# Kernel tuning notes

Hardware: AMD Instinct MI355X
Metric: run time of the kernel (lower is better)

## Reference

```python
import jax, jax.numpy as jnp
import numpy as np

BETA = 0.9
THRESHOLD = 1.0
SLOPE = 25.0  # snntorch fast_sigmoid default slope
T_STEPS = 64
IN_DIM, HID, NCLS = 256, 128, 8
BATCH = 16384


@jax.custom_vjp
def spike(u):
    # heaviside(u) with fast_sigmoid surrogate gradient
    return (u > 0).astype(u.dtype)

def _spike_fwd(u):
    return spike(u), u

def _spike_bwd(u, g):
    return (g / (SLOPE * jnp.abs(u) + 1.0) ** 2,)

spike.defvjp(_spike_fwd, _spike_bwd)


def setup_inputs() -> dict:
    key = jax.random.key(0)
    k1, k2, k3, k4, k5 = jax.random.split(key, 5)
    b1_bound = 1.0 / np.sqrt(IN_DIM)
    b2_bound = 1.0 / np.sqrt(HID)
    return {
        "x": jax.random.normal(k1, (BATCH, IN_DIM), jnp.float32),
        "W1": jax.random.uniform(k2, (HID, IN_DIM), jnp.float32, -b1_bound, b1_bound),
        "b1": jax.random.uniform(k3, (HID,), jnp.float32, -b1_bound, b1_bound),
        "W2": jax.random.uniform(k4, (NCLS, HID), jnp.float32, -b2_bound, b2_bound),
        "b2": jax.random.uniform(k5, (NCLS,), jnp.float32, -b2_bound, b2_bound),
    }


def reference(x, W1, b1, W2, b2):
    # fc1(x) is identical every timestep -> hoist out of the loop (same math)
    cur1 = x @ W1.T + b1  # [B, HID]

    def step(carry, _):
        mem1, mem2, acc = carry
        # snntorch Leaky (reset_mechanism='subtract'):
        # reset computed from incoming mem, detached
        reset1 = jax.lax.stop_gradient((mem1 - THRESHOLD > 0).astype(mem1.dtype))
        mem1 = BETA * mem1 + cur1 - reset1 * THRESHOLD
        spk1 = spike(mem1 - THRESHOLD)

        cur2 = spk1 @ W2.T + b2  # [B, NCLS]
        reset2 = jax.lax.stop_gradient((mem2 - THRESHOLD > 0).astype(mem2.dtype))
        mem2 = BETA * mem2 + cur2 - reset2 * THRESHOLD
        spk2 = spike(mem2 - THRESHOLD)
        return (mem1, mem2, acc + spk2), None

    mem1_0 = jnp.zeros((x.shape[0], HID), x.dtype)
    mem2_0 = jnp.zeros((x.shape[0], NCLS), x.dtype)
    acc0 = jnp.zeros((x.shape[0], NCLS), x.dtype)
    (_, _, out), _ = jax.lax.scan(step, (mem1_0, mem2_0, acc0), None, length=T_STEPS)
    return out
```

## Files before the change

kernel.cpp:

```cpp
#include <hip/hip_runtime.h>
#include <math.h>


#define T_STEPS 64
#define IN_DIM  256
#define HID     128
#define NCLS    8

#define ROWS   32
#define THR    256
#define A_KQ   16
#define RSTR   260

typedef float f32x4 __attribute__((ext_vector_type(4)));

static __device__ __forceinline__ unsigned int pkspk(float a, float b) {
    auto h = __builtin_amdgcn_cvt_pkrtz(a, b);
    return __builtin_bit_cast(unsigned int, h);
}

__global__ __launch_bounds__(THR, 2)
void snn_fused(const float* __restrict__ x, const float* __restrict__ W1,
               const float* __restrict__ b1, const float* __restrict__ W2,
               const float* __restrict__ b2, float* __restrict__ out)
{
#pragma clang fp contract(off)
    __shared__ __align__(16) char smem[33280];
    float4 (* const w1c)[HID + 2] = (float4 (*)[HID + 2])smem;
    unsigned int* const pk  = (unsigned int*)smem;
    float*        const wsl = (float*)smem;

    const int tid  = threadIdx.x;
    const int lane = tid & 63;

    {
        const int wv = __builtin_amdgcn_readfirstlane(tid >> 6);
        const size_t rowg0 = (size_t)blockIdx.x * ROWS;
        const float* xb = x + (rowg0 + (size_t)wv * 8) * IN_DIM;

        float accL[8], accH[8];
        #pragma unroll
        for (int j = 0; j < 8; ++j) { accL[j] = 0.0f; accH[j] = 0.0f; }

        #pragma unroll 1
        for (int ch = 0; ch < 4; ++ch) {
            const int kbase = ch * (A_KQ * 4);
            #pragma unroll
            for (int s = 0; s < 8; ++s) {
                const int idx = tid + s * THR;
                const int h = idx >> 4, kq = idx & 15;
                w1c[kq][h] = *(const float4*)(W1 + (size_t)h * IN_DIM + kbase + kq * 4);
            }
            __syncthreads();

            const float* xbc = xb + kbase;
            #pragma unroll 4
            for (int kq = 0; kq < A_KQ; ++kq) {
                const float* xkq = xbc + kq * 4;
                f32x4 q0, q1, q2, q3, q4, q5, q6, q7;
                asm volatile(
                    "s_load_dwordx4 %0, %8, 0x0\n\t"
                    "s_load_dwordx4 %1, %8, 0x400\n\t"
                    "s_load_dwordx4 %2, %8, 0x800\n\t"
                    "s_load_dwordx4 %3, %8, 0xc00\n\t"
                    "s_load_dwordx4 %4, %8, 0x1000\n\t"
                    "s_load_dwordx4 %5, %8, 0x1400\n\t"
                    "s_load_dwordx4 %6, %8, 0x1800\n\t"
                    "s_load_dwordx4 %7, %8, 0x1c00\n\t"
                    "s_waitcnt lgkmcnt(0)"
                    : "=&s"(q0), "=&s"(q1), "=&s"(q2), "=&s"(q3),
                      "=&s"(q4), "=&s"(q5), "=&s"(q6), "=&s"(q7)
                    : "s"(xkq));

                const float4 wL = w1c[kq][lane];
                const float4 wH = w1c[kq][64 + lane];
#define ROWFMA(J, XQ) { \
                float aL = accL[J], aH = accH[J]; \
                aL = fmaf(XQ.x, wL.x, aL); \
                aL = fmaf(XQ.y, wL.y, aL); \
                aL = fmaf(XQ.z, wL.z, aL); \
                aL = fmaf(XQ.w, wL.w, aL); \
                aH = fmaf(XQ.x, wH.x, aH); \
                aH = fmaf(XQ.y, wH.y, aH); \
                aH = fmaf(XQ.z, wH.z, aH); \
                aH = fmaf(XQ.w, wH.w, aH); \
                accL[J] = aL; accH[J] = aH; }
                ROWFMA(0, q0) ROWFMA(1, q1) ROWFMA(2, q2) ROWFMA(3, q3)
                ROWFMA(4, q4) ROWFMA(5, q5) ROWFMA(6, q6) ROWFMA(7, q7)
#undef ROWFMA
            }
            __syncthreads();
        }

        const float bL = b1[lane], bH = b1[64 + lane];
        #pragma unroll
        for (int j = 0; j < 8; ++j) {
            const int rr = wv * 8 + j;
            wsl[rr * HID + lane]      = accL[j] + bL;
            wsl[rr * HID + 64 + lane] = accH[j] + bH;
        }
    }

    const int r = tid >> 3;
    const int q = tid & 7;

    const int brow = lane & 31;
    const int bcls = 2 * (tid >> 6) + (lane >> 5);
    const float b2c = b2[bcls];

    float4 w2r[32];
    {
        const float4* wg = (const float4*)(W2 + bcls * HID);
        #pragma unroll
        for (int g = 0; g < 32; ++g) w2r[g] = wg[g];
    }

    __syncthreads();

    float cur1[16];
    {
        const float* src = wsl + r * HID + q * 16;
        #pragma unroll
        for (int i = 0; i < 4; ++i) {
            const float4 v = *(const float4*)(src + 4 * i);
            cur1[4*i+0] = v.x; cur1[4*i+1] = v.y;
            cur1[4*i+2] = v.z; cur1[4*i+3] = v.w;
        }
    }
    __syncthreads();

    float mem1[16], spk1[16];
    #pragma unroll
    for (int i = 0; i < 16; ++i) { mem1[i] = 0.0f; spk1[i] = 0.0f; }
    float m2 = 0.0f, r2v = 0.0f, o = 0.0f;

    #pragma unroll 1
    for (int ts = 0; ts < T_STEPS; ts += 4) {
        #pragma unroll
        for (int j = 0; j < 4; ++j) {
            #pragma unroll
            for (int i = 0; i < 16; ++i) {
                float tmp = 0.9f * mem1[i];
                tmp = tmp + cur1[i];
                float m = tmp - spk1[i];
                mem1[i] = m;
                spk1[i] = (m > 1.0f) ? 1.0f : 0.0f;
            }
            unsigned int* dst = &pk[r * RSTR + j * 64 + q * 8];
            #pragma unroll
            for (int s = 0; s < 2; ++s) {
                uint4 pv;
                pv.x = pkspk(spk1[8*s+0], spk1[8*s+1]);
                pv.y = pkspk(spk1[8*s+2], spk1[8*s+3]);
                pv.z = pkspk(spk1[8*s+4], spk1[8*s+5]);
                pv.w = pkspk(spk1[8*s+6], spk1[8*s+7]);
                *(uint4*)(dst + 4 * s) = pv;
            }
        }
        __syncthreads();

        float a0 = 0.0f, a1 = 0.0f, a2 = 0.0f, a3 = 0.0f;
        const unsigned int* src = &pk[brow * RSTR];
#define FMIX_LO(A, P, W) \
        asm("v_fma_mix_f32 %0, %1, %2, %0 op_sel_hi:[1,0,0]" \
            : "+v"(A) : "v"(P), "v"(W));
#define FMIX_HI(A, P, W) \
        asm("v_fma_mix_f32 %0, %1, %2, %0 op_sel:[1,0,0] op_sel_hi:[1,0,0]" \
            : "+v"(A) : "v"(P), "v"(W));
#define TR(A, P) \
        FMIX_LO(A, P.x, wA.x) FMIX_HI(A, P.x, wA.y) \
        FMIX_LO(A, P.y, wA.z) FMIX_HI(A, P.y, wA.w) \
        FMIX_LO(A, P.z, wB.x) FMIX_HI(A, P.z, wB.y) \
        FMIX_LO(A, P.w, wB.z) FMIX_HI(A, P.w, wB.w)
        #pragma unroll
        for (int gg = 0; gg < 16; ++gg) {
            const float4 wA = w2r[2 * gg];
            const float4 wB = w2r[2 * gg + 1];
            const uint4 p0 = *(const uint4*)(src + 0 * 64 + 4 * gg);
            const uint4 p1 = *(const uint4*)(src + 1 * 64 + 4 * gg);
            const uint4 p2 = *(const uint4*)(src + 2 * 64 + 4 * gg);
            const uint4 p3 = *(const uint4*)(src + 3 * 64 + 4 * gg);
            TR(a0, p0) TR(a1, p1) TR(a2, p2) TR(a3, p3)
        }
#undef TR
#undef FMIX_HI
#undef FMIX_LO
        __syncthreads();

        const float aa[4] = {a0, a1, a2, a3};
        #pragma unroll
        for (int j = 0; j < 4; ++j) {
            const float c2 = aa[j] + b2c;
            float t2 = 0.9f * m2; t2 = t2 + c2; m2 = t2 - r2v;
            r2v = (m2 > 1.0f) ? 1.0f : 0.0f;
            o = o + r2v;
        }
    }

    out[((size_t)blockIdx.x * ROWS + brow) * NCLS + bcls] = o;
}

extern "C" void kernel_launch(void* const* d_in, const int* in_sizes, int n_in,
                              void* d_out, int out_size, void* d_ws, size_t ws_size,
                              hipStream_t stream) {
    const float* x  = (const float*)d_in[0];
    const float* W1 = (const float*)d_in[1];
    const float* b1 = (const float*)d_in[2];
    const float* W2 = (const float*)d_in[3];
    const float* b2 = (const float*)d_in[4];
    float* out = (float*)d_out;
    (void)d_ws; (void)ws_size;

    const int batch = in_sizes[0] / IN_DIM;
    snn_fused<<<batch / ROWS, THR, 0, stream>>>(x, W1, b1, W2, b2, out);
}
```

Before: 144.6 us.

## Halve rows per block, stage W2 in LDS, split layer-2 timesteps across lane halves

Each block now handles 16 rows instead of 32, and the launch bound asks for 4 blocks per CU instead of 2. Per-thread state shrinks from 16 to 8 hidden neurons, and the 32-register W2 row cache moves into shared memory. The layer-2 reduction splits the four timesteps between lane halves, which exchange results with a cross-lane shuffle, and only half the lanes write output. The aim is lower register pressure and higher occupancy to hide latency. The cost is twice as many blocks, W1 reloaded per block, extra LDS reads of W2, and a shuffle each step.

```diff
diff --git a/kernel.cpp b/kernel.cpp
--- a/kernel.cpp
+++ b/kernel.cpp
@@ -7,7 +7,7 @@
 #define HID     128
 #define NCLS    8
 
-#define ROWS   32
+#define ROWS   16
 #define THR    256
 #define A_KQ   16
 #define RSTR   260
@@ -19,7 +19,7 @@
     return __builtin_bit_cast(unsigned int, h);
 }
 
-__global__ __launch_bounds__(THR, 2)
+__global__ __launch_bounds__(THR, 4)
 void snn_fused(const float* __restrict__ x, const float* __restrict__ W1,
                const float* __restrict__ b1, const float* __restrict__ W2,
                const float* __restrict__ b2, float* __restrict__ out)
@@ -28,6 +28,7 @@
     __shared__ __align__(16) char smem[33280];
     float4 (* const w1c)[HID + 2] = (float4 (*)[HID + 2])smem;
     unsigned int* const pk  = (unsigned int*)smem;
+    float4*       const w2l = (float4*)(smem + 16640);
     float*        const wsl = (float*)smem;
 
     const int tid  = threadIdx.x;
@@ -36,11 +37,11 @@
     {
         const int wv = __builtin_amdgcn_readfirstlane(tid >> 6);
         const size_t rowg0 = (size_t)blockIdx.x * ROWS;
-        const float* xb = x + (rowg0 + (size_t)wv * 8) * IN_DIM;
-
-        float accL[8], accH[8];
-        #pragma unroll
-        for (int j = 0; j < 8; ++j) { accL[j] = 0.0f; accH[j] = 0.0f; }
+        const float* xb = x + (rowg0 + (size_t)wv * 4) * IN_DIM;
+
+        float accL[4], accH[4];
+        #pragma unroll
+        for (int j = 0; j < 4; ++j) { accL[j] = 0.0f; accH[j] = 0.0f; }
 
         #pragma unroll 1
         for (int ch = 0; ch < 4; ++ch) {
@@ -57,19 +58,14 @@
             #pragma unroll 4
             for (int kq = 0; kq < A_KQ; ++kq) {
                 const float* xkq = xbc + kq * 4;
-                f32x4 q0, q1, q2, q3, q4, q5, q6, q7;
+                f32x4 q0, q1, q2, q3;
                 asm volatile(
-                    "s_load_dwordx4 %0, %8, 0x0\n\t"
-                    "s_load_dwordx4 %1, %8, 0x400\n\t"
-                    "s_load_dwordx4 %2, %8, 0x800\n\t"
-                    "s_load_dwordx4 %3, %8, 0xc00\n\t"
-                    "s_load_dwordx4 %4, %8, 0x1000\n\t"
-                    "s_load_dwordx4 %5, %8, 0x1400\n\t"
-                    "s_load_dwordx4 %6, %8, 0x1800\n\t"
-                    "s_load_dwordx4 %7, %8, 0x1c00\n\t"
+                    "s_load_dwordx4 %0, %4, 0x0\n\t"
+                    "s_load_dwordx4 %1, %4, 0x400\n\t"
+                    "s_load_dwordx4 %2, %4, 0x800\n\t"
+                    "s_load_dwordx4 %3, %4, 0xc00\n\t"
                     "s_waitcnt lgkmcnt(0)"
-                    : "=&s"(q0), "=&s"(q1), "=&s"(q2), "=&s"(q3),
-                      "=&s"(q4), "=&s"(q5), "=&s"(q6), "=&s"(q7)
+                    : "=&s"(q0), "=&s"(q1), "=&s"(q2), "=&s"(q3)
                     : "s"(xkq));
 
                 const float4 wL = w1c[kq][lane];
@@ -86,7 +82,6 @@
                 aH = fmaf(XQ.w, wH.w, aH); \
                 accL[J] = aL; accH[J] = aH; }
                 ROWFMA(0, q0) ROWFMA(1, q1) ROWFMA(2, q2) ROWFMA(3, q3)
-                ROWFMA(4, q4) ROWFMA(5, q5) ROWFMA(6, q6) ROWFMA(7, q7)
 #undef ROWFMA
             }
             __syncthreads();
@@ -94,34 +89,23 @@
 
         const float bL = b1[lane], bH = b1[64 + lane];
         #pragma unroll
-        for (int j = 0; j < 8; ++j) {
-            const int rr = wv * 8 + j;
+        for (int j = 0; j < 4; ++j) {
+            const int rr = wv * 4 + j;
             wsl[rr * HID + lane]      = accL[j] + bL;
             wsl[rr * HID + 64 + lane] = accH[j] + bH;
         }
+        w2l[tid] = ((const float4*)W2)[tid];
     }
-
-    const int r = tid >> 3;
-    const int q = tid & 7;
-
-    const int brow = lane & 31;
-    const int bcls = 2 * (tid >> 6) + (lane >> 5);
-    const float b2c = b2[bcls];
-
-    float4 w2r[32];
+    __syncthreads();
+
+    const int r = tid >> 4;
+    const int q = tid & 15;
+
+    float cur1[8];
     {
-        const float4* wg = (const float4*)(W2 + bcls * HID);
-        #pragma unroll
-        for (int g = 0; g < 32; ++g) w2r[g] = wg[g];
-    }
-
-    __syncthreads();
-
-    float cur1[16];
-    {
-        const float* src = wsl + r * HID + q * 16;
-        #pragma unroll
-        for (int i = 0; i < 4; ++i) {
+        const float* src = wsl + r * HID + q * 8;
+        #pragma unroll
+        for (int i = 0; i < 2; ++i) {
             const float4 v = *(const float4*)(src + 4 * i);
             cur1[4*i+0] = v.x; cur1[4*i+1] = v.y;
             cur1[4*i+2] = v.z; cur1[4*i+3] = v.w;
@@ -129,9 +113,16 @@
     }
     __syncthreads();
 
-    float mem1[16], spk1[16];
+    const int brow  = lane & 15;
+    const int u     = lane >> 4;
+    const bool hihalf = (lane >= 32);
+    const int bcls  = 2 * (tid >> 6) + (u & 1);
+    const float b2c = b2[bcls];
+    const float4* __restrict__ w2p = &w2l[bcls * 32];
+
+    float mem1[8], spk1[8];
     #pragma unroll
-    for (int i = 0; i < 16; ++i) { mem1[i] = 0.0f; spk1[i] = 0.0f; }
+    for (int i = 0; i < 8; ++i) { mem1[i] = 0.0f; spk1[i] = 0.0f; }
     float m2 = 0.0f, r2v = 0.0f, o = 0.0f;
 
     #pragma unroll 1
@@ -139,28 +130,24 @@
         #pragma unroll
         for (int j = 0; j < 4; ++j) {
             #pragma unroll
-            for (int i = 0; i < 16; ++i) {
+            for (int i = 0; i < 8; ++i) {
                 float tmp = 0.9f * mem1[i];
                 tmp = tmp + cur1[i];
                 float m = tmp - spk1[i];
                 mem1[i] = m;
                 spk1[i] = (m > 1.0f) ? 1.0f : 0.0f;
             }
-            unsigned int* dst = &pk[r * RSTR + j * 64 + q * 8];
-            #pragma unroll
-            for (int s = 0; s < 2; ++s) {
-                uint4 pv;
-                pv.x = pkspk(spk1[8*s+0], spk1[8*s+1]);
-                pv.y = pkspk(spk1[8*s+2], spk1[8*s+3]);
-                pv.z = pkspk(spk1[8*s+4], spk1[8*s+5]);
-                pv.w = pkspk(spk1[8*s+6], spk1[8*s+7]);
-                *(uint4*)(dst + 4 * s) = pv;
-            }
+            uint4 pv;
+            pv.x = pkspk(spk1[0], spk1[1]);
+            pv.y = pkspk(spk1[2], spk1[3]);
+            pv.z = pkspk(spk1[4], spk1[5]);
+            pv.w = pkspk(spk1[6], spk1[7]);
+            *(uint4*)(&pk[r * RSTR + j * 64 + q * 4]) = pv;
         }
         __syncthreads();
 
-        float a0 = 0.0f, a1 = 0.0f, a2 = 0.0f, a3 = 0.0f;
-        const unsigned int* src = &pk[brow * RSTR];
+        float aE = 0.0f, aF = 0.0f;
+        const unsigned int* srcT = &pk[brow * RSTR + (hihalf ? 128 : 0)];
 #define FMIX_LO(A, P, W) \
         asm("v_fma_mix_f32 %0, %1, %2, %0 op_sel_hi:[1,0,0]" \
             : "+v"(A) : "v"(P), "v"(W));
@@ -174,30 +161,35 @@
         FMIX_LO(A, P.w, wB.z) FMIX_HI(A, P.w, wB.w)
         #pragma unroll
         for (int gg = 0; gg < 16; ++gg) {
-            const float4 wA = w2r[2 * gg];
-            const float4 wB = w2r[2 * gg + 1];
-            const uint4 p0 = *(const uint4*)(src + 0 * 64 + 4 * gg);
-            const uint4 p1 = *(const uint4*)(src + 1 * 64 + 4 * gg);
-            const uint4 p2 = *(const uint4*)(src + 2 * 64 + 4 * gg);
-            const uint4 p3 = *(const uint4*)(src + 3 * 64 + 4 * gg);
-            TR(a0, p0) TR(a1, p1) TR(a2, p2) TR(a3, p3)
+            const float4 wA = w2p[2 * gg];
+            const float4 wB = w2p[2 * gg + 1];
+            const uint4 ra = *(const uint4*)(srcT + 4 * gg);
+            const uint4 rb = *(const uint4*)(srcT + 64 + 4 * gg);
+            TR(aE, ra) TR(aF, rb)
         }
 #undef TR
 #undef FMIX_HI
 #undef FMIX_LO
         __syncthreads();
 
-        const float aa[4] = {a0, a1, a2, a3};
+        const float pE = __shfl_xor(aE, 32, 64);
+        const float pF = __shfl_xor(aF, 32, 64);
+        const float t0 = hihalf ? pE : aE;
+        const float t1 = hihalf ? pF : aF;
+        const float t2 = hihalf ? aE : pE;
+        const float t3 = hihalf ? aF : pF;
+        const float aa[4] = {t0, t1, t2, t3};
         #pragma unroll
         for (int j = 0; j < 4; ++j) {
             const float c2 = aa[j] + b2c;
-            float t2 = 0.9f * m2; t2 = t2 + c2; m2 = t2 - r2v;
+            float tt = 0.9f * m2; tt = tt + c2; m2 = tt - r2v;
             r2v = (m2 > 1.0f) ? 1.0f : 0.0f;
             o = o + r2v;
         }
     }
 
-    out[((size_t)blockIdx.x * ROWS + brow) * NCLS + bcls] = o;
+    if (lane < 32)
+        out[((size_t)blockIdx.x * ROWS + brow) * NCLS + bcls] = o;
 }
 
 extern "C" void kernel_launch(void* const* d_in, const int* in_sizes, int n_in,
```

New measurement: 152.6 us. 1.05x slower.

## Double-buffer spike LDS buffer to overlap layer-1 update with layer-2 matvec

Applied to the files above, without the earlier changes.

Splits the packed spike buffer in shared memory into two halves and software-pipelines the time loop. Each iteration writes the next four timesteps' layer-1 spikes into one buffer while reading the current buffer for the layer-2 reduction, which halves the barriers per iteration. The cost is doubling LDS use to about 65 KB per block, which at launch bounds of two blocks per CU may lower occupancy. It also adds a prologue and a buffer-select branch.

```diff
diff --git a/kernel.cpp b/kernel.cpp
--- a/kernel.cpp
+++ b/kernel.cpp
@@ -25,9 +25,10 @@
                const float* __restrict__ b2, float* __restrict__ out)
 {
 #pragma clang fp contract(off)
-    __shared__ __align__(16) char smem[33280];
+    __shared__ __align__(16) char smem[66560];
     float4 (* const w1c)[HID + 2] = (float4 (*)[HID + 2])smem;
-    unsigned int* const pk  = (unsigned int*)smem;
+    unsigned int* const pkA = (unsigned int*)smem;
+    unsigned int* const pkB = (unsigned int*)(smem + 33280);
     float*        const wsl = (float*)smem;
 
     const int tid  = threadIdx.x;
@@ -134,33 +135,41 @@
     for (int i = 0; i < 16; ++i) { mem1[i] = 0.0f; spk1[i] = 0.0f; }
     float m2 = 0.0f, r2v = 0.0f, o = 0.0f;
 
+#define PHASE_A(BUF) \
+    _Pragma("unroll") \
+    for (int j = 0; j < 4; ++j) { \
+        _Pragma("unroll") \
+        for (int i = 0; i < 16; ++i) { \
+            float tmp = 0.9f * mem1[i];    \
+            tmp = tmp + cur1[i];           \
+            float m = tmp - spk1[i];       \
+            mem1[i] = m; \
+            spk1[i] = (m > 1.0f) ? 1.0f : 0.0f; \
+        } \
+        unsigned int* dst = &(BUF)[r * RSTR + j * 64 + q * 8]; \
+        _Pragma("unroll") \
+        for (int s = 0; s < 2; ++s) { \
+            uint4 pv; \
+            pv.x = pkspk(spk1[8*s+0], spk1[8*s+1]); \
+            pv.y = pkspk(spk1[8*s+2], spk1[8*s+3]); \
+            pv.z = pkspk(spk1[8*s+4], spk1[8*s+5]); \
+            pv.w = pkspk(spk1[8*s+6], spk1[8*s+7]); \
+            *(uint4*)(dst + 4 * s) = pv; \
+        } \
+    }
+
+    PHASE_A(pkA);
+    __syncthreads();
+
     #pragma unroll 1
-    for (int ts = 0; ts < T_STEPS; ts += 4) {
-        #pragma unroll
-        for (int j = 0; j < 4; ++j) {
-            #pragma unroll
-            for (int i = 0; i < 16; ++i) {
-                float tmp = 0.9f * mem1[i];
-                tmp = tmp + cur1[i];
-                float m = tmp - spk1[i];
-                mem1[i] = m;
-                spk1[i] = (m > 1.0f) ? 1.0f : 0.0f;
-            }
-            unsigned int* dst = &pk[r * RSTR + j * 64 + q * 8];
-            #pragma unroll
-            for (int s = 0; s < 2; ++s) {
-                uint4 pv;
-                pv.x = pkspk(spk1[8*s+0], spk1[8*s+1]);
-                pv.y = pkspk(spk1[8*s+2], spk1[8*s+3]);
-                pv.z = pkspk(spk1[8*s+4], spk1[8*s+5]);
-                pv.w = pkspk(spk1[8*s+6], spk1[8*s+7]);
-                *(uint4*)(dst + 4 * s) = pv;
-            }
-        }
-        __syncthreads();
+    for (int g = 0; g < 16; ++g) {
+        unsigned int* const curb = (g & 1) ? pkB : pkA;
+        unsigned int* const nxtb = (g & 1) ? pkA : pkB;
+
+        if (g < 15) { PHASE_A(nxtb); }
 
         float a0 = 0.0f, a1 = 0.0f, a2 = 0.0f, a3 = 0.0f;
-        const unsigned int* src = &pk[brow * RSTR];
+        const unsigned int* src = &curb[brow * RSTR];
 #define FMIX_LO(A, P, W) \
         asm("v_fma_mix_f32 %0, %1, %2, %0 op_sel_hi:[1,0,0]" \
             : "+v"(A) : "v"(P), "v"(W));
@@ -185,6 +194,7 @@
 #undef TR
 #undef FMIX_HI
 #undef FMIX_LO
+
         __syncthreads();
 
         const float aa[4] = {a0, a1, a2, a3};
@@ -196,6 +206,7 @@
             o = o + r2v;
         }
     }
+#undef PHASE_A
 
     out[((size_t)blockIdx.x * ROWS + brow) * NCLS + bcls] = o;
 }
```

Measured after the change: 148.3 us. 2.5% more time.
